# Performance work log

Hardware: AMD Instinct MI355X
Metric: run time of the kernel (lower is better)

## Reference

```python
import jax, jax.numpy as jnp
import numpy as np

NEG_SLOPE = 0.2  # PyG GATConv leaky_relu slope


def _gat_conv(x, src, dst, W, a_s, a_d, b, H, D, concat):
    """PyG-style GATConv (eval mode, self-loops already in src/dst).
    x: [N, F_in], W: [F_in, H*D], a_s/a_d: [H, D], b: [H*D] or [D]."""
    N = x.shape[0]
    h = (x @ W).reshape(N, H, D)                      # [N, H, D]
    al_src = (h * a_s).sum(-1)                        # [N, H]
    al_dst = (h * a_d).sum(-1)                        # [N, H]
    e = jax.nn.leaky_relu(al_src[src] + al_dst[dst], NEG_SLOPE)   # [E, H]
    m = jax.ops.segment_max(e, dst, num_segments=N)               # [N, H]
    m = jnp.where(jnp.isfinite(m), m, 0.0)
    ex = jnp.exp(e - m[dst])
    denom = jax.ops.segment_sum(ex, dst, num_segments=N)
    alpha = ex / (denom[dst] + 1e-16)                 # edge softmax per dst node
    out = jax.ops.segment_sum(alpha[:, :, None] * h[src], dst, num_segments=N)  # [N, H, D]
    out = out.reshape(N, H * D) if concat else out.mean(axis=1)
    return out + b


def setup_inputs() -> dict:
    key = jax.random.key(0)
    ks = jax.random.split(key, 14)
    N, E, F_in, H, D, OUT = 50000, 800000, 256, 8, 32, 64
    g = lambda k, shape, fan: (jax.random.normal(k, shape, jnp.float32) / np.float32(np.sqrt(fan)))
    return {
        "x": jax.random.normal(ks[0], (N, F_in), jnp.float32),
        "edge_index": jax.random.randint(ks[1], (2, E), 0, N),
        # conv0: GATConv(256 -> 32, heads=8, concat)
        "W0": g(ks[2], (F_in, H * D), F_in),
        "a_src0": g(ks[3], (H, D), D),
        "a_dst0": g(ks[4], (H, D), D),
        "b0": jnp.zeros((H * D,), jnp.float32),
        # residual0: Linear(256 -> 256)
        "Wr0": g(ks[5], (F_in, H * D), F_in),
        "br0": jnp.zeros((H * D,), jnp.float32),
        # conv1: GATConv(256 -> 64, heads=1, concat=False)
        "W1": g(ks[6], (H * D, OUT), H * D),
        "a_src1": g(ks[7], (1, OUT), OUT),
        "a_dst1": g(ks[8], (1, OUT), OUT),
        "b1": jnp.zeros((OUT,), jnp.float32),
        # residual1: Linear(256 -> 64)
        "Wr1": g(ks[9], (H * D, OUT), H * D),
        "br1": jnp.zeros((OUT,), jnp.float32),
    }


def reference(x, edge_index, W0, a_src0, a_dst0, b0, Wr0, br0, W1, a_src1, a_dst1, b1, Wr1, br1):
    N = x.shape[0]
    loops = jnp.arange(N, dtype=edge_index.dtype)
    src = jnp.concatenate([edge_index[0], loops])   # add self loops
    dst = jnp.concatenate([edge_index[1], loops])
    # layer 0: GATConv + residual + ELU (dropout is identity in eval)
    h = _gat_conv(x, src, dst, W0, a_src0, a_dst0, b0, 8, 32, True)
    h = jax.nn.elu(h + (x @ Wr0 + br0))
    # final layer: heads=1, concat=False, + residual
    out = _gat_conv(h, src, dst, W1, a_src1, a_dst1, b1, 1, 64, False)
    out = out + (h @ Wr1 + br1)
    return jax.nn.log_softmax(out, axis=1)
```

## Files before the change

kernel.cpp:

```cpp
#include <hip/hip_runtime.h>
#include <math.h>

#define NEG_SLOPE 0.2f
#define BSH 7
#define NBLK_PART 256

typedef __attribute__((ext_vector_type(8))) short bf16x8;
typedef __attribute__((ext_vector_type(4))) float f32x4;
typedef __attribute__((ext_vector_type(2))) float f32x2;
typedef __attribute__((ext_vector_type(8))) unsigned short ushort8;
typedef __attribute__((ext_vector_type(4))) unsigned short ushort4v;

__device__ __forceinline__ float b2f(unsigned short u){
  return __uint_as_float(((unsigned)u) << 16);
}
__device__ __forceinline__ unsigned short f2b(float f){
  unsigned u = __float_as_uint(f);
  return (unsigned short)((u + 0x7FFFu + ((u >> 16) & 1u)) >> 16);
}

#if __has_builtin(__builtin_amdgcn_cvt_pk_f32_fp8) && __has_builtin(__builtin_amdgcn_cvt_pk_fp8_f32)
#define HW_FP8 1
#else
#define HW_FP8 0
#endif

#if !HW_FP8
__device__ __forceinline__ unsigned enc8_one(float f){
  unsigned bits = __float_as_uint(f);
  unsigned s = bits >> 31;
  unsigned e = (bits >> 23) & 255;
  unsigned mant = bits & 0x7FFFFF;
  if(e < 121){
    float af = fabsf(f);
    int m = (int)(af * 512.f + 0.5f);
    if(m > 7) m = 7;
    return (s << 7) | (unsigned)m;
  }
  unsigned lsb = (mant >> 20) & 1;
  mant += 0x7FFFF + lsb;
  if(mant >> 23){ e += 1; mant = 0; }
  unsigned m3 = mant >> 20;
  unsigned e8 = e - 120;
  if(e8 > 15 || (e8 == 15 && m3 == 7)) return (s << 7) | 0x7E;
  return (s << 7) | (e8 << 3) | m3;
}
#endif

template<bool HI>
__device__ __forceinline__ unsigned enc8_pair(float a, float b, unsigned old){
#if HW_FP8
  return __builtin_amdgcn_cvt_pk_fp8_f32(a, b, old, HI);
#else
  unsigned p = enc8_one(a) | (enc8_one(b) << 8);
  return HI ? ((old & 0x0000FFFFu) | (p << 16)) : ((old & 0xFFFF0000u) | p);
#endif
}

__device__ __forceinline__ unsigned char enc8b(float v){
  return (unsigned char)(enc8_pair<false>(v, v, 0u) & 0xFFu);
}

__device__ __forceinline__ void dec8x4v(unsigned q, f32x2& lo, f32x2& hi){
#if HW_FP8
  lo = __builtin_amdgcn_cvt_pk_f32_fp8(q, false);
  hi = __builtin_amdgcn_cvt_pk_f32_fp8(q, true);
#else
  auto dec1 = [](unsigned b)->float{
    unsigned s = (b >> 7) & 1, e = (b >> 3) & 15, m = b & 7;
    float v = (e == 0) ? (float)m * 0.001953125f
                       : __uint_as_float(((e + 120) << 23) | (m << 20));
    return s ? -v : v;
  };
  lo[0] = dec1(q & 255); lo[1] = dec1((q >> 8) & 255);
  hi[0] = dec1((q >> 16) & 255); hi[1] = dec1(q >> 24);
#endif
}

extern "C" __global__ void k_part1(const int* __restrict__ dsts, int E, int N,
                                   int NBUCK, int* __restrict__ bcnt,
                                   int* __restrict__ blockbase){
  __shared__ int hist[512];
  int blk = blockIdx.x, tid = threadIdx.x;
  for(int b = tid; b < NBUCK; b += 256) hist[b] = 0;
  __syncthreads();
  int ET = E + N;
  int chunk = (ET + NBLK_PART - 1)/NBLK_PART;
  int s0 = blk*chunk, s1 = s0+chunk < ET ? s0+chunk : ET;
  for(int e = s0+tid; e < s1; e += 256){
    int d = (e < E) ? dsts[e] : e - E;
    atomicAdd(&hist[d >> BSH], 1);
  }
  __syncthreads();
  for(int b = tid; b < NBUCK; b += 256)
    blockbase[(size_t)blk*NBUCK + b] = atomicAdd(&bcnt[b], hist[b]);
}

extern "C" __global__ void k_bscan(const int* __restrict__ bcnt, int* __restrict__ boffs,
                                   int* __restrict__ offs_last, int NBUCK, int ET){
  __shared__ int sc[512], orig[512];
  int t = threadIdx.x;
  int v = (t < NBUCK) ? bcnt[t] : 0;
  sc[t] = v; orig[t] = v;
  __syncthreads();
  for(int st=1; st<512; st<<=1){
    int u = (t >= st) ? sc[t-st] : 0;
    __syncthreads();
    sc[t] += u;
    __syncthreads();
  }
  if(t < NBUCK) boffs[t] = sc[t] - orig[t];
  if(t == 0){ boffs[NBUCK] = ET; *offs_last = ET; }
}

extern "C" __global__ void k_part2(const int* __restrict__ srcs, const int* __restrict__ dsts,
                                   int E, int N, int NBUCK,
                                   const int* __restrict__ boffs, const int* __restrict__ blockbase,
                                   uint2* __restrict__ pairs){
  __shared__ int cur[512];
  int blk = blockIdx.x, tid = threadIdx.x;
  for(int b = tid; b < NBUCK; b += 256)
    cur[b] = boffs[b] + blockbase[(size_t)blk*NBUCK + b];
  __syncthreads();
  int ET = E + N;
  int chunk = (ET + NBLK_PART - 1)/NBLK_PART;
  int s0 = blk*chunk, s1 = s0+chunk < ET ? s0+chunk : ET;
  for(int e = s0+tid; e < s1; e += 256){
    int s, d;
    if(e < E){ s = srcs[e]; d = dsts[e]; } else { s = d = e - E; }
    int pos = atomicAdd(&cur[d >> BSH], 1);
    uint2 pr; pr.x = (unsigned)d; pr.y = (unsigned)s;
    pairs[pos] = pr;
  }
}

extern "C" __global__ void k_bcsr(const uint2* __restrict__ pairs, const int* __restrict__ boffs,
                                  int N, int* __restrict__ offs, int* __restrict__ csr){
  __shared__ int hist[128], sc[128], lcur[128];
  int b = blockIdx.x, tid = threadIdx.x;
  int node0 = b << BSH;
  int base = boffs[b], endp = boffs[b+1];
  if(tid < 128) hist[tid] = 0;
  __syncthreads();
  for(int i = base + tid; i < endp; i += 256)
    atomicAdd(&hist[pairs[i].x & 127], 1);
  __syncthreads();
  if(tid < 128) sc[tid] = hist[tid];
  __syncthreads();
  for(int st=1; st<128; st<<=1){
    int u = (tid < 128 && tid >= st) ? sc[tid-st] : 0;
    __syncthreads();
    if(tid < 128) sc[tid] += u;
    __syncthreads();
  }
  if(tid < 128){
    int ex = sc[tid] - hist[tid];
    lcur[tid] = ex;
    int n = node0 + tid;
    if(n < N) offs[n] = base + ex;
  }
  __syncthreads();
  for(int i = base + tid; i < endp; i += 256){
    uint2 pr = pairs[i];
    int pos = atomicAdd(&lcur[pr.x & 127], 1);
    csr[base + pos] = (int)pr.y;
  }
}

extern "C" __global__ void k_cast_x(const float* __restrict__ x, unsigned short* __restrict__ xb, int n8){
  int i = blockIdx.x*blockDim.x + threadIdx.x;
  if(i >= n8) return;
  const float4* p = (const float4*)(x + (size_t)i*8);
  float4 v0 = p[0], v1 = p[1];
  ushort8 o;
  o[0]=f2b(v0.x); o[1]=f2b(v0.y); o[2]=f2b(v0.z); o[3]=f2b(v0.w);
  o[4]=f2b(v1.x); o[5]=f2b(v1.y); o[6]=f2b(v1.z); o[7]=f2b(v1.w);
  *(ushort8*)(xb + (size_t)i*8) = o;
}

extern "C" __global__ void k_wt2(const float* __restrict__ W0, const float* __restrict__ Wr0,
                                 const float* __restrict__ W1, const float* __restrict__ Wr1,
                                 unsigned short* __restrict__ WT0, unsigned short* __restrict__ WT1){
  int idx = blockIdx.x*256 + threadIdx.x;
  const int tot0 = 512*256;
  if(idx < tot0){
    int n = idx >> 8, k = idx & 255;
    const float* W = (n < 256) ? W0 : Wr0;
    int c = (n < 256) ? n : n - 256;
    WT0[idx] = f2b(W[(size_t)k*256 + c]);
  } else {
    idx -= tot0;
    if(idx >= 128*256) return;
    int n = idx >> 8, k = idx & 255;
    const float* W = (n < 64) ? W1 : Wr1;
    int c = (n < 64) ? n : n - 64;
    WT1[idx] = f2b(W[(size_t)k*64 + c]);
  }
}

__launch_bounds__(256)
extern "C" __global__ void k_mgemm(const unsigned short* __restrict__ A,
                                   const unsigned short* __restrict__ WT,
                                   unsigned short* __restrict__ C, int ldc, int M,
                                   int MB, int NCB, unsigned char* __restrict__ qout){
  int id = blockIdx.x;
  int row_blk, col_blk;
  if(NCB == 4){
    int group = id >> 5;
    int r8 = id & 7;
    col_blk = (id >> 3) & 3;
    row_blk = group*8 + r8;
  } else {
    row_blk = id; col_blk = 0;
  }
  if(row_blk >= MB) return;

  __shared__ unsigned short As[128*64];
  __shared__ unsigned short Bs[128*64];
  int t = threadIdx.x;
  int lane = t & 63, wid = t >> 6;
  int wr = wid >> 1, wc = wid & 1;
  int row0 = row_blk*128, col0 = col_blk*128;
  f32x4 acc[4][4] = {};

  for(int k0 = 0; k0 < 256; k0 += 64){
    #pragma unroll
    for(int i=0; i<4; i++){
      int t2 = i*256 + t;
      int r = t2 >> 3;
      int dslot = (t2 & 7) ^ (r & 7);
      int gr = row0 + r; if(gr >= M) gr = M - 1;
      const unsigned short* ga = A + (size_t)gr*256 + k0 + dslot*8;
      __builtin_amdgcn_global_load_lds((const __attribute__((address_space(1))) unsigned*)ga,
          (__attribute__((address_space(3))) unsigned*)(As + i*2048 + wid*512), 16, 0, 0);
      const unsigned short* gb = WT + (size_t)(col0 + r)*256 + k0 + dslot*8;
      __builtin_amdgcn_global_load_lds((const __attribute__((address_space(1))) unsigned*)gb,
          (__attribute__((address_space(3))) unsigned*)(Bs + i*2048 + wid*512), 16, 0, 0);
    }
    __syncthreads();
    #pragma unroll
    for(int kc=0; kc<2; kc++){
      bf16x8 a[4], b[4];
      int kb = kc*4 + (lane >> 4);
      #pragma unroll
      for(int f=0; f<4; f++){
        int ar = wr*64 + f*16 + (lane & 15);
        a[f] = *(const bf16x8*)&As[ar*64 + ((kb ^ (ar & 7))*8)];
        int br = wc*64 + f*16 + (lane & 15);
        b[f] = *(const bf16x8*)&Bs[br*64 + ((kb ^ (br & 7))*8)];
      }
      #pragma unroll
      for(int fm=0; fm<4; fm++)
        #pragma unroll
        for(int fn=0; fn<4; fn++)
          acc[fm][fn] = __builtin_amdgcn_mfma_f32_16x16x32_bf16(a[fm], b[fn], acc[fm][fn], 0, 0, 0);
    }
    __syncthreads();
  }

  int rb = row0 + wr*64 + ((lane >> 4) << 2);
  int cb = col0 + wc*64 + (lane & 15);
  #pragma unroll
  for(int fm=0; fm<4; fm++){
    #pragma unroll
    for(int r=0; r<4; r++){
      int row = rb + fm*16 + r;
      if(row < M){
        #pragma unroll
        for(int fn=0; fn<4; fn++)
          C[(size_t)row*ldc + cb + fn*16] = f2b(acc[fm][fn][r]);
        if(qout){
          #pragma unroll
          for(int fn=0; fn<4; fn++){
            int col = cb + fn*16;
            if(col < 256) qout[(size_t)row*256 + col] = enc8b(acc[fm][fn][r]);
          }
        }
      }
    }
  }
}

extern "C" __global__ void k_al0(const unsigned short* __restrict__ buf0b, const float* __restrict__ as0,
                                 const float* __restrict__ ad0, float* als0, float* ald0, int N){
  int i = blockIdx.x*blockDim.x + threadIdx.x;
  if(i >= N*8) return;
  int n = i >> 3, h = i & 7;
  const uint4* hp = (const uint4*)(buf0b + (size_t)n*512 + h*32);
  const float* av = as0 + h*32;
  const float* dv = ad0 + h*32;
  float s = 0.f, d = 0.f;
  #pragma unroll
  for(int q=0; q<4; q++){
    uint4 u = hp[q];
    unsigned w[4] = {u.x, u.y, u.z, u.w};
    #pragma unroll
    for(int j=0; j<4; j++){
      float lo = __uint_as_float(w[j] << 16);
      float hi = __uint_as_float(w[j] & 0xFFFF0000u);
      int c = q*8 + j*2;
      s += lo*av[c] + hi*av[c+1];
      d += lo*dv[c] + hi*dv[c+1];
    }
  }
  als0[i] = s; ald0[i] = d;
}

__launch_bounds__(256)
extern "C" __global__ void k_gather0(const unsigned short* __restrict__ buf0b,
                                     const unsigned char* __restrict__ h0q,
                                     const float* __restrict__ als0, const float* __restrict__ ald0,
                                     const int* __restrict__ offs, const int* __restrict__ csr,
                                     const float* __restrict__ b0, const float* __restrict__ br0,
                                     unsigned short* __restrict__ h1b, int N){
  int n = blockIdx.x*4 + (threadIdx.x >> 6);
  if(n >= N) return;
  int lane = threadIdx.x & 63;
  int hh = lane & 7;
  int es = lane >> 3;
  int h  = es;
  int c  = lane*4;
  float ald_h = ald0[n*8 + hh];
  int beg = offs[n], end = offs[n+1];

  f32x2 A01 = {0.f, 0.f}, A23 = {0.f, 0.f};
  float den = 0.f;

  for(int chunk = beg; chunk < end; chunk += 8){
    int m = end - chunk; if(m > 8) m = 8;
    bool e_ok = es < m;
    int s = e_ok ? csr[chunk + es] : 0;
    float p = 0.f;
    if(e_ok){
      float v = als0[s*8 + hh] + ald_h;
      v = v > 0.f ? v : NEG_SLOPE*v;
      p = expf(v);
    }
    den += p;
    int sj[8]; float pj[8];
    #pragma unroll
    for(int j=0; j<8; j++){
      sj[j] = __shfl(s, j*8);
      pj[j] = __shfl(p, j*8 + h);
    }
    unsigned q[8];
    #pragma unroll
    for(int j=0; j<8; j++)
      q[j] = *(const unsigned*)(h0q + (size_t)sj[j]*256 + c);
    #pragma unroll
    for(int j=0; j<8; j++){
      f32x2 lo, hi, pv;
      dec8x4v(q[j], lo, hi);
      pv[0] = pj[j]; pv[1] = pj[j];
      A01 += pv*lo; A23 += pv*hi;
    }
  }

  den += __shfl_xor(den, 8);
  den += __shfl_xor(den, 16);
  den += __shfl_xor(den, 32);
  float rden = 1.f/(den + 1e-16f);
  rden = __shfl(rden, h);

  float a0 = A01[0]*rden, a1 = A01[1]*rden, a2 = A23[0]*rden, a3 = A23[1]*rden;

  float4 bb = *(const float4*)(b0 + c);
  float4 rb = *(const float4*)(br0 + c);
  uint2 ru = *(const uint2*)(buf0b + (size_t)n*512 + 256 + c);
  float o0 = a0 + bb.x + __uint_as_float(ru.x << 16)         + rb.x;
  float o1 = a1 + bb.y + __uint_as_float(ru.x & 0xFFFF0000u) + rb.y;
  float o2 = a2 + bb.z + __uint_as_float(ru.y << 16)         + rb.z;
  float o3 = a3 + bb.w + __uint_as_float(ru.y & 0xFFFF0000u) + rb.w;
  ushort4v o;
  o[0] = f2b(o0 > 0.f ? o0 : expf(o0) - 1.f);
  o[1] = f2b(o1 > 0.f ? o1 : expf(o1) - 1.f);
  o[2] = f2b(o2 > 0.f ? o2 : expf(o2) - 1.f);
  o[3] = f2b(o3 > 0.f ? o3 : expf(o3) - 1.f);
  *(ushort4v*)(h1b + (size_t)n*256 + c) = o;
}

extern "C" __global__ void k_al1(const unsigned short* __restrict__ buf1b, const float* __restrict__ as1,
                                 const float* __restrict__ ad1, float* als1, float* ald1, int N){
  int n = blockIdx.x*4 + (threadIdx.x >> 6);
  if(n >= N) return;
  int lane = threadIdx.x & 63;
  float g = b2f(buf1b[(size_t)n*128 + lane]);
  float s = g*as1[lane], d = g*ad1[lane];
  #pragma unroll
  for(int o=32; o>0; o>>=1){ s += __shfl_xor(s,o); d += __shfl_xor(d,o); }
  if(lane == 0){ als1[n] = s; ald1[n] = d; }
}

__launch_bounds__(256)
extern "C" __global__ void k_gather1(const unsigned short* __restrict__ buf1b,
                                     const float* __restrict__ als1, const float* __restrict__ ald1,
                                     const int* __restrict__ offs, const int* __restrict__ csr,
                                     const float* __restrict__ b1, const float* __restrict__ br1,
                                     float* __restrict__ out, int N){
  int n = blockIdx.x*4 + (threadIdx.x >> 6);
  if(n >= N) return;
  int lane = threadIdx.x & 63;
  int ch2 = lane & 31;
  int es  = lane >> 5;
  int beg = offs[n], end = offs[n+1];
  float ald_n = ald1[n];

  f32x2 acc = {0.f, 0.f};
  float den = 0.f;

  for(int chunk = beg; chunk < end; chunk += 64){
    int m = end - chunk; if(m > 64) m = 64;
    int s = (lane < m) ? csr[chunk + lane] : 0;
    float p = 0.f;
    if(lane < m){
      float v = als1[s] + ald_n;
      v = v > 0.f ? v : NEG_SLOPE*v;
      p = expf(v);
    }
    den += p;
    for(int base = 0; base < m; base += 8){
      int sv[4]; float pv[4];
      #pragma unroll
      for(int i=0; i<4; i++){
        int j = base + 2*i + es;
        int jj = j & 63;
        int   sx = __shfl(s, jj);
        float px = __shfl(p, jj);
        bool ok = j < m;
        sv[i] = ok ? sx : 0;
        pv[i] = ok ? px : 0.f;
      }
      unsigned uv[4];
      #pragma unroll
      for(int i=0; i<4; i++)
        uv[i] = *(const unsigned*)(buf1b + (size_t)sv[i]*128 + ch2*2);
      #pragma unroll
      for(int i=0; i<4; i++){
        f32x2 f, pp;
        f[0] = __uint_as_float(uv[i] << 16);
        f[1] = __uint_as_float(uv[i] & 0xFFFF0000u);
        pp[0] = pv[i]; pp[1] = pv[i];
        acc += pp*f;
      }
    }
  }

  acc[0] += __shfl_xor(acc[0], 32);
  acc[1] += __shfl_xor(acc[1], 32);
  #pragma unroll
  for(int o=32; o>0; o>>=1) den += __shfl_xor(den, o);
  float rden = 1.f/(den + 1e-16f);
  acc[0] *= rden; acc[1] *= rden;

  float2 bb = *(const float2*)(b1 + ch2*2);
  float2 rb = *(const float2*)(br1 + ch2*2);
  unsigned ru = *(const unsigned*)(buf1b + (size_t)n*128 + 64 + ch2*2);
  float vx = acc[0] + bb.x + __uint_as_float(ru << 16)         + rb.x;
  float vy = acc[1] + bb.y + __uint_as_float(ru & 0xFFFF0000u) + rb.y;

  float mx = fmaxf(vx, vy);
  #pragma unroll
  for(int o=16; o>0; o>>=1) mx = fmaxf(mx, __shfl_xor(mx, o));
  float sm = expf(vx - mx) + expf(vy - mx);
  #pragma unroll
  for(int o=16; o>0; o>>=1) sm += __shfl_xor(sm, o);
  float l = mx + logf(sm);
  if(es == 0){
    float2 ov; ov.x = vx - l; ov.y = vy - l;
    *(float2*)(out + (size_t)n*64 + ch2*2) = ov;
  }
}

extern "C" void kernel_launch(void* const* d_in, const int* in_sizes, int n_in,
                              void* d_out, int out_size, void* d_ws, size_t ws_size,
                              hipStream_t stream){
  const float* x   = (const float*)d_in[0];
  const int*   ei  = (const int*)  d_in[1];
  const float* W0  = (const float*)d_in[2];
  const float* as0 = (const float*)d_in[3];
  const float* ad0 = (const float*)d_in[4];
  const float* b0  = (const float*)d_in[5];
  const float* Wr0 = (const float*)d_in[6];
  const float* br0 = (const float*)d_in[7];
  const float* W1  = (const float*)d_in[8];
  const float* as1 = (const float*)d_in[9];
  const float* ad1 = (const float*)d_in[10];
  const float* b1  = (const float*)d_in[11];
  const float* Wr1 = (const float*)d_in[12];
  const float* br1 = (const float*)d_in[13];
  int N = in_sizes[0] / 256;
  int E = in_sizes[1] / 2;
  const int* srcs = ei;
  const int* dsts = ei + E;
  float* out = (float*)d_out;

  int ET = E + N;
  int NBUCK = (N + 127) >> BSH;

  unsigned short* buf0b = (unsigned short*)d_ws;
  unsigned short* xb    = buf0b + (size_t)N*512;
  unsigned short* h1b   = xb    + (size_t)N*256;
  unsigned short* buf1b = h1b   + (size_t)N*256;
  unsigned short* WT0   = buf1b + (size_t)N*128;
  unsigned short* WT1   = WT0   + 512*256;
  float*    als0 = (float*)(WT1 + 128*256);
  float*    ald0 = als0 + (size_t)N*8;
  float*    als1 = ald0 + (size_t)N*8;
  float*    ald1 = als1 + N;
  int*      offs = (int*)(ald1 + N);
  int*      bcnt = offs + N + 1;
  int*      boffs = bcnt + NBUCK;
  int*      blockbase = boffs + NBUCK + 1;
  int*      csr  = blockbase + (size_t)NBLK_PART*NBUCK;
  uint2*    pairs = (uint2*)(csr + ET);
  pairs = (uint2*)(((uintptr_t)pairs + 7) & ~(uintptr_t)7);
  unsigned char* h0q = (unsigned char*)xb;

  hipMemsetAsync(bcnt, 0, (size_t)NBUCK*sizeof(int), stream);
  hipLaunchKernelGGL(k_part1, dim3(NBLK_PART), dim3(256), 0, stream, dsts, E, N, NBUCK, bcnt, blockbase);
  hipLaunchKernelGGL(k_bscan, dim3(1), dim3(512), 0, stream, bcnt, boffs, offs + N, NBUCK, ET);
  hipLaunchKernelGGL(k_part2, dim3(NBLK_PART), dim3(256), 0, stream, srcs, dsts, E, N, NBUCK, boffs, blockbase, pairs);
  hipLaunchKernelGGL(k_bcsr, dim3(NBUCK), dim3(256), 0, stream, pairs, boffs, N, offs, csr);

  int n8 = N*256/8;
  hipLaunchKernelGGL(k_cast_x, dim3((n8+255)/256), dim3(256), 0, stream, x, xb, n8);
  hipLaunchKernelGGL(k_wt2, dim3((512*256+128*256+255)/256), dim3(256), 0, stream, W0, Wr0, W1, Wr1, WT0, WT1);

  int MB = (N + 127) / 128;
  int g0 = ((MB + 7) / 8) * 32;
  hipLaunchKernelGGL(k_mgemm, dim3(g0), dim3(256), 0, stream, xb, WT0, buf0b, 512, N, MB, 4, h0q);
  hipLaunchKernelGGL(k_al0, dim3((N*8+255)/256), dim3(256), 0, stream, buf0b, as0, ad0, als0, ald0, N);
  hipLaunchKernelGGL(k_gather0, dim3((N+3)/4), dim3(256), 0, stream, buf0b, h0q, als0, ald0, offs, csr, b0, br0, h1b, N);

  hipLaunchKernelGGL(k_mgemm, dim3(MB), dim3(256), 0, stream, h1b, WT1, buf1b, 128, N, MB, 1, (unsigned char*)nullptr);
  hipLaunchKernelGGL(k_al1, dim3((N+3)/4), dim3(256), 0, stream, buf1b, as1, ad1, als1, ald1, N);
  hipLaunchKernelGGL(k_gather1, dim3((N+3)/4), dim3(256), 0, stream, buf1b, als1, ald1, offs, csr, b1, br1, out, N);
}
```

Baseline: 208.5 us.

## Fuse fp32-to-bf16 cast into first GEMM and gather layer-1 from 8-bit features

Removes the separate cast kernel: the first GEMM now reads fp32 x directly, converts it to bf16 in registers and writes the result to shared memory instead of using direct global-to-LDS loads. The second GEMM also emits an 8-bit quantized copy of the layer-1 features, and gather1 reads these 4-byte packed values (4 channels per lane, 16 edges per step) instead of bf16 pairs, halving gather traffic. In exchange, the first GEMM loses the async LDS load path for A and layer-1 aggregation uses lower-precision features. The edge-validity masking in the gather loop was also removed and relies on p being zero for inactive lanes.

```diff
diff --git a/kernel.cpp b/kernel.cpp
--- a/kernel.cpp
+++ b/kernel.cpp
@@ -165,17 +165,6 @@
     int pos = atomicAdd(&lcur[pr.x & 127], 1);
     csr[base + pos] = (int)pr.y;
   }
-}
-
-extern "C" __global__ void k_cast_x(const float* __restrict__ x, unsigned short* __restrict__ xb, int n8){
-  int i = blockIdx.x*blockDim.x + threadIdx.x;
-  if(i >= n8) return;
-  const float4* p = (const float4*)(x + (size_t)i*8);
-  float4 v0 = p[0], v1 = p[1];
-  ushort8 o;
-  o[0]=f2b(v0.x); o[1]=f2b(v0.y); o[2]=f2b(v0.z); o[3]=f2b(v0.w);
-  o[4]=f2b(v1.x); o[5]=f2b(v1.y); o[6]=f2b(v1.z); o[7]=f2b(v1.w);
-  *(ushort8*)(xb + (size_t)i*8) = o;
 }
 
 extern "C" __global__ void k_wt2(const float* __restrict__ W0, const float* __restrict__ Wr0,
@@ -200,9 +189,11 @@
 
 __launch_bounds__(256)
 extern "C" __global__ void k_mgemm(const unsigned short* __restrict__ A,
+                                   const float* __restrict__ Afp,
                                    const unsigned short* __restrict__ WT,
                                    unsigned short* __restrict__ C, int ldc, int M,
-                                   int MB, int NCB, unsigned char* __restrict__ qout){
+                                   int MB, int NCB,
+                                   unsigned char* __restrict__ qout, int qcols){
   int id = blockIdx.x;
   int row_blk, col_blk;
   if(NCB == 4){
@@ -224,15 +215,38 @@
   f32x4 acc[4][4] = {};
 
   for(int k0 = 0; k0 < 256; k0 += 64){
+    if(Afp){
+      #pragma unroll
+      for(int i=0; i<4; i++){
+        int t2 = i*256 + t;
+        int r = t2 >> 3;
+        int dslot = (t2 & 7) ^ (r & 7);
+        int gr = row0 + r; if(gr >= M) gr = M - 1;
+        const float* ga = Afp + (size_t)gr*256 + k0 + dslot*8;
+        float4 v0 = *(const float4*)ga;
+        float4 v1 = *(const float4*)(ga + 4);
+        ushort8 o;
+        o[0]=f2b(v0.x); o[1]=f2b(v0.y); o[2]=f2b(v0.z); o[3]=f2b(v0.w);
+        o[4]=f2b(v1.x); o[5]=f2b(v1.y); o[6]=f2b(v1.z); o[7]=f2b(v1.w);
+        *(ushort8*)(As + i*2048 + wid*512 + lane*8) = o;
+      }
+    } else {
+      #pragma unroll
+      for(int i=0; i<4; i++){
+        int t2 = i*256 + t;
+        int r = t2 >> 3;
+        int dslot = (t2 & 7) ^ (r & 7);
+        int gr = row0 + r; if(gr >= M) gr = M - 1;
+        const unsigned short* ga = A + (size_t)gr*256 + k0 + dslot*8;
+        __builtin_amdgcn_global_load_lds((const __attribute__((address_space(1))) unsigned*)ga,
+            (__attribute__((address_space(3))) unsigned*)(As + i*2048 + wid*512), 16, 0, 0);
+      }
+    }
     #pragma unroll
     for(int i=0; i<4; i++){
       int t2 = i*256 + t;
       int r = t2 >> 3;
       int dslot = (t2 & 7) ^ (r & 7);
-      int gr = row0 + r; if(gr >= M) gr = M - 1;
-      const unsigned short* ga = A + (size_t)gr*256 + k0 + dslot*8;
-      __builtin_amdgcn_global_load_lds((const __attribute__((address_space(1))) unsigned*)ga,
-          (__attribute__((address_space(3))) unsigned*)(As + i*2048 + wid*512), 16, 0, 0);
       const unsigned short* gb = WT + (size_t)(col0 + r)*256 + k0 + dslot*8;
       __builtin_amdgcn_global_load_lds((const __attribute__((address_space(1))) unsigned*)gb,
           (__attribute__((address_space(3))) unsigned*)(Bs + i*2048 + wid*512), 16, 0, 0);
@@ -273,7 +287,7 @@
           #pragma unroll
           for(int fn=0; fn<4; fn++){
             int col = cb + fn*16;
-            if(col < 256) qout[(size_t)row*256 + col] = enc8b(acc[fm][fn][r]);
+            if(col < qcols) qout[(size_t)row*qcols + col] = enc8b(acc[fm][fn][r]);
           }
         }
       }
@@ -393,6 +407,7 @@
 
 __launch_bounds__(256)
 extern "C" __global__ void k_gather1(const unsigned short* __restrict__ buf1b,
+                                     const unsigned char* __restrict__ g1q,
                                      const float* __restrict__ als1, const float* __restrict__ ald1,
                                      const int* __restrict__ offs, const int* __restrict__ csr,
                                      const float* __restrict__ b1, const float* __restrict__ br1,
@@ -400,12 +415,13 @@
   int n = blockIdx.x*4 + (threadIdx.x >> 6);
   if(n >= N) return;
   int lane = threadIdx.x & 63;
-  int ch2 = lane & 31;
-  int es  = lane >> 5;
+  int ch4 = lane & 15;
+  int es  = lane >> 4;
+  int c   = ch4*4;
   int beg = offs[n], end = offs[n+1];
   float ald_n = ald1[n];
 
-  f32x2 acc = {0.f, 0.f};
+  f32x2 A01 = {0.f, 0.f}, A23 = {0.f, 0.f};
   float den = 0.f;
 
   for(int chunk = beg; chunk < end; chunk += 64){
@@ -418,56 +434,55 @@
       p = expf(v);
     }
     den += p;
-    for(int base = 0; base < m; base += 8){
+    for(int base = 0; base < m; base += 16){
       int sv[4]; float pv[4];
       #pragma unroll
       for(int i=0; i<4; i++){
-        int j = base + 2*i + es;
+        int j = base + 4*i + es;
         int jj = j & 63;
-        int   sx = __shfl(s, jj);
-        float px = __shfl(p, jj);
-        bool ok = j < m;
-        sv[i] = ok ? sx : 0;
-        pv[i] = ok ? px : 0.f;
+        sv[i] = __shfl(s, jj);
+        pv[i] = __shfl(p, jj);
       }
-      unsigned uv[4];
+      unsigned qv[4];
       #pragma unroll
       for(int i=0; i<4; i++)
-        uv[i] = *(const unsigned*)(buf1b + (size_t)sv[i]*128 + ch2*2);
+        qv[i] = *(const unsigned*)(g1q + (size_t)sv[i]*64 + c);
       #pragma unroll
       for(int i=0; i<4; i++){
-        f32x2 f, pp;
-        f[0] = __uint_as_float(uv[i] << 16);
-        f[1] = __uint_as_float(uv[i] & 0xFFFF0000u);
+        f32x2 lo, hi, pp;
+        dec8x4v(qv[i], lo, hi);
         pp[0] = pv[i]; pp[1] = pv[i];
-        acc += pp*f;
+        A01 += pp*lo; A23 += pp*hi;
       }
     }
   }
 
-  acc[0] += __shfl_xor(acc[0], 32);
-  acc[1] += __shfl_xor(acc[1], 32);
+  A01[0] += __shfl_xor(A01[0], 16); A01[1] += __shfl_xor(A01[1], 16);
+  A23[0] += __shfl_xor(A23[0], 16); A23[1] += __shfl_xor(A23[1], 16);
+  A01[0] += __shfl_xor(A01[0], 32); A01[1] += __shfl_xor(A01[1], 32);
+  A23[0] += __shfl_xor(A23[0], 32); A23[1] += __shfl_xor(A23[1], 32);
   #pragma unroll
   for(int o=32; o>0; o>>=1) den += __shfl_xor(den, o);
   float rden = 1.f/(den + 1e-16f);
-  acc[0] *= rden; acc[1] *= rden;
-
-  float2 bb = *(const float2*)(b1 + ch2*2);
-  float2 rb = *(const float2*)(br1 + ch2*2);
-  unsigned ru = *(const unsigned*)(buf1b + (size_t)n*128 + 64 + ch2*2);
-  float vx = acc[0] + bb.x + __uint_as_float(ru << 16)         + rb.x;
-  float vy = acc[1] + bb.y + __uint_as_float(ru & 0xFFFF0000u) + rb.y;
-
-  float mx = fmaxf(vx, vy);
+
+  float4 bb = *(const float4*)(b1 + c);
+  float4 rb = *(const float4*)(br1 + c);
+  uint2 ru = *(const uint2*)(buf1b + (size_t)n*128 + 64 + c);
+  float v0 = A01[0]*rden + bb.x + __uint_as_float(ru.x << 16)         + rb.x;
+  float v1 = A01[1]*rden + bb.y + __uint_as_float(ru.x & 0xFFFF0000u) + rb.y;
+  float v2 = A23[0]*rden + bb.z + __uint_as_float(ru.y << 16)         + rb.z;
+  float v3 = A23[1]*rden + bb.w + __uint_as_float(ru.y & 0xFFFF0000u) + rb.w;
+
+  float mx = fmaxf(fmaxf(v0, v1), fmaxf(v2, v3));
   #pragma unroll
-  for(int o=16; o>0; o>>=1) mx = fmaxf(mx, __shfl_xor(mx, o));
-  float sm = expf(vx - mx) + expf(vy - mx);
+  for(int o=1; o<16; o<<=1) mx = fmaxf(mx, __shfl_xor(mx, o));
+  float sm = expf(v0-mx) + expf(v1-mx) + expf(v2-mx) + expf(v3-mx);
   #pragma unroll
-  for(int o=16; o>0; o>>=1) sm += __shfl_xor(sm, o);
+  for(int o=1; o<16; o<<=1) sm += __shfl_xor(sm, o);
   float l = mx + logf(sm);
   if(es == 0){
-    float2 ov; ov.x = vx - l; ov.y = vy - l;
-    *(float2*)(out + (size_t)n*64 + ch2*2) = ov;
+    float4 ov; ov.x = v0-l; ov.y = v1-l; ov.z = v2-l; ov.w = v3-l;
+    *(float4*)(out + (size_t)n*64 + c) = ov;
   }
 }
 
@@ -514,6 +529,7 @@
   int*      csr  = blockbase + (size_t)NBLK_PART*NBUCK;
   uint2*    pairs = (uint2*)(csr + ET);
   pairs = (uint2*)(((uintptr_t)pairs + 7) & ~(uintptr_t)7);
+  unsigned char* g1q = (unsigned char*)(pairs + ET);
   unsigned char* h0q = (unsigned char*)xb;
 
   hipMemsetAsync(bcnt, 0, (size_t)NBUCK*sizeof(int), stream);
@@ -522,17 +538,17 @@
   hipLaunchKernelGGL(k_part2, dim3(NBLK_PART), dim3(256), 0, stream, srcs, dsts, E, N, NBUCK, boffs, blockbase, pairs);
   hipLaunchKernelGGL(k_bcsr, dim3(NBUCK), dim3(256), 0, stream, pairs, boffs, N, offs, csr);
 
-  int n8 = N*256/8;
-  hipLaunchKernelGGL(k_cast_x, dim3((n8+255)/256), dim3(256), 0, stream, x, xb, n8);
   hipLaunchKernelGGL(k_wt2, dim3((512*256+128*256+255)/256), dim3(256), 0, stream, W0, Wr0, W1, Wr1, WT0, WT1);
 
   int MB = (N + 127) / 128;
   int g0 = ((MB + 7) / 8) * 32;
-  hipLaunchKernelGGL(k_mgemm, dim3(g0), dim3(256), 0, stream, xb, WT0, buf0b, 512, N, MB, 4, h0q);
+  hipLaunchKernelGGL(k_mgemm, dim3(g0), dim3(256), 0, stream,
+                     (const unsigned short*)nullptr, x, WT0, buf0b, 512, N, MB, 4, h0q, 256);
   hipLaunchKernelGGL(k_al0, dim3((N*8+255)/256), dim3(256), 0, stream, buf0b, as0, ad0, als0, ald0, N);
   hipLaunchKernelGGL(k_gather0, dim3((N+3)/4), dim3(256), 0, stream, buf0b, h0q, als0, ald0, offs, csr, b0, br0, h1b, N);
 
-  hipLaunchKernelGGL(k_mgemm, dim3(MB), dim3(256), 0, stream, h1b, WT1, buf1b, 128, N, MB, 1, (unsigned char*)nullptr);
+  hipLaunchKernelGGL(k_mgemm, dim3(MB), dim3(256), 0, stream,
+                     h1b, (const float*)nullptr, WT1, buf1b, 128, N, MB, 1, g1q, 64);
   hipLaunchKernelGGL(k_al1, dim3((N+3)/4), dim3(256), 0, stream, buf1b, as1, ad1, als1, ald1, N);
-  hipLaunchKernelGGL(k_gather1, dim3((N+3)/4), dim3(256), 0, stream, buf1b, als1, ald1, offs, csr, b1, br1, out, N);
-}
+  hipLaunchKernelGGL(k_gather1, dim3((N+3)/4), dim3(256), 0, stream, buf1b, g1q, als1, ald1, offs, csr, b1, br1, out, N);
+}
```

Result: faster. 201.6 us (-3.3%).
